# Kernel tuning notes

Hardware: AMD Instinct MI355X
Metric: run time of the kernel (lower is better)

The kernel has to match this reference:

```python
import jax, jax.numpy as jnp
import numpy as np

POOLED = 7          # square pooled grid (grid_width == grid_height required by torch_combined_meshgrid)
NUM_LEVELS = 6      # len_feature_maps; level = clamp(floor(5 + log2(sqrt(w*h))), 0, 5)


def _bilinear_sample(fm, gx, gy):
    """fm: [C, D, D]; gx, gy: [N, G, G] normalized coords in [0,1].
    Faithful to getWeightedSum_ofFourFmapPoints: floor/ceil corner points with
    proportion weights; coord dim 0 (x) indexes fmap rows, dim 1 (y) indexes cols.
    Returns [N, C, G, G]."""
    D = fm.shape[-1]
    ux = gx * (D - 1)
    uy = gy * (D - 1)
    x0 = jnp.floor(ux); x1 = jnp.ceil(ux)
    y0 = jnp.floor(uy); y1 = jnp.ceil(uy)
    ddx = jnp.where(x1 - x0 == 0, 1.0, x1 - x0)
    ddy = jnp.where(y1 - y0 == 0, 1.0, y1 - y0)
    px0 = 1.0 - (ux - x0) / ddx   # proportion_to_take_from_start_x
    px1 = 1.0 - px0
    py0 = 1.0 - (uy - y0) / ddy
    py1 = 1.0 - py0
    ix0 = x0.astype(jnp.int32); ix1 = x1.astype(jnp.int32)
    iy0 = y0.astype(jnp.int32); iy1 = y1.astype(jnp.int32)
    # advanced indexing: fm[:, idx, idx] -> [C, N, G, G]
    tl = fm[:, ix0, iy0]
    tr = fm[:, ix1, iy0]
    bl = fm[:, ix0, iy1]
    br = fm[:, ix1, iy1]
    w_tl = (px0 * py0)[None]
    w_tr = (px1 * py0)[None]
    w_bl = (px0 * py1)[None]
    w_br = (px1 * py1)[None]
    pooled = w_tl * tl + w_tr * tr + w_bl * bl + w_br * br  # [C, N, G, G]
    return jnp.moveaxis(pooled, 0, 1)                        # [N, C, G, G]


def setup_inputs() -> dict:
    key = jax.random.key(0)
    N, C = 2000, 256
    dims = [38, 19, 10, 5, 3, 1]
    kw, kh, kx, ky, *kf = jax.random.split(key, 4 + len(dims))
    w = jax.random.uniform(kw, (N, 1), minval=0.02, maxval=0.98)
    h = jax.random.uniform(kh, (N, 1), minval=0.02, maxval=0.98)
    x1 = jax.random.uniform(kx, (N, 1)) * (1.0 - w)
    y1 = jax.random.uniform(ky, (N, 1)) * (1.0 - h)
    boxes = jnp.concatenate([x1, y1, x1 + w, y1 + h], axis=1)  # x1 y1 x2 y2 in [0,1]
    out = {"boxes": boxes}
    for i, (d, k) in enumerate(zip(dims, kf)):
        out[f"fmap{i}"] = jax.random.normal(k, (1, C, d, d), dtype=jnp.float32)
    return out


def reference(boxes, fmap0, fmap1, fmap2, fmap3, fmap4, fmap5):
    fmaps = [fmap0, fmap1, fmap2, fmap3, fmap4, fmap5]
    N = boxes.shape[0]
    C = fmap0.shape[1]
    G = POOLED
    x1, y1, x2, y2 = boxes[:, 0:1], boxes[:, 1:2], boxes[:, 2:3], boxes[:, 3:4]
    # FPN-style level index: floor(5 + log2(sqrt(w*h))), clamped (constant w.r.t. grad)
    avg = jnp.sqrt((x2 - x1) * (y2 - y1))
    lvl = jnp.clip(jnp.floor((NUM_LEVELS - 1.0) + jnp.log2(avg)), 0, NUM_LEVELS - 1)
    lvl = jax.lax.stop_gradient(lvl.astype(jnp.int32).reshape(-1))  # [N]
    # bilinear interpolation grid: grid[n,i,j] = (x1 + i*dx/(G-1), y1 + j*dy/(G-1)), clamped
    t = jnp.arange(G, dtype=boxes.dtype)
    denom = max(1.0, G - 1.0)
    xr = jnp.clip(x1 + t[None, :] * (x2 - x1) / denom, 0.0, 1.0)  # [N, G]
    yr = jnp.clip(y1 + t[None, :] * (y2 - y1) / denom, 0.0, 1.0)  # [N, G]
    gx = jnp.broadcast_to(xr[:, :, None], (N, G, G))
    gy = jnp.broadcast_to(yr[:, None, :], (N, G, G))
    out = jnp.zeros((N, C, G, G), dtype=fmap0.dtype)
    for l, f in enumerate(fmaps):
        fm = f[0]  # [C, D, D] (single image; one fmap selected per box)
        if fm.shape[-1] == 1:
            # original returns fmap[:, :, 0:1, 0:1]; broadcast the constant to the grid
            pooled = jnp.broadcast_to(fm[None, :, :1, :1], (N, C, G, G))
        else:
            pooled = _bilinear_sample(fm, gx, gy)
        mask = (lvl == l).astype(fmap0.dtype)[:, None, None, None]
        out = out + mask * pooled
    return out
```

## Files before the change

### kernel.cpp

```cpp
#include <hip/hip_runtime.h>

#define G 7
#define CCH 256
#define NLVL 6

__device__ __constant__ int kD[NLVL]  = {38, 19, 10, 5, 3, 1};
__device__ __constant__ int kD2[NLVL] = {1444, 361, 100, 25, 9, 1};
__device__ __constant__ int kBaseT[NLVL + 1] = {0, 369664, 462080, 487680, 494080, 496384, 496640};

#define FMT_TOTAL 496640

__global__ __launch_bounds__(256) void transpose_fmaps(
    const float* __restrict__ f0, const float* __restrict__ f1,
    const float* __restrict__ f2, const float* __restrict__ f3,
    const float* __restrict__ f4, const float* __restrict__ f5,
    float* __restrict__ fmT)
{
    int o = blockIdx.x * blockDim.x + threadIdx.x;
    if (o >= FMT_TOTAL) return;
    int l = 0;
#pragma unroll
    for (int k = 1; k < NLVL; ++k) l += (o >= kBaseT[k]);
    int rel = o - kBaseT[l];
    int p = rel >> 8;
    int c = rel & 255;
    const float* f;
    switch (l) {
        case 0: f = f0; break;
        case 1: f = f1; break;
        case 2: f = f2; break;
        case 3: f = f3; break;
        case 4: f = f4; break;
        default: f = f5; break;
    }
    fmT[o] = f[c * kD2[l] + p];
}

__global__ __launch_bounds__(256) void roialign_main(
    const float* __restrict__ boxes, const float* __restrict__ fmT,
    float* __restrict__ out)
{
    __shared__ float sOut[CCH * 49];
    __shared__ float4 sW[49];
    __shared__ int4 sOff[49];

    int n = blockIdx.x;
    int tid = threadIdx.x;

    if (tid < 49) {
        float bx1 = boxes[n * 4 + 0];
        float by1 = boxes[n * 4 + 1];
        float bx2 = boxes[n * 4 + 2];
        float by2 = boxes[n * 4 + 3];
        float w = bx2 - bx1;
        float h = by2 - by1;
        float avg = sqrtf(w * h);
        float lf = floorf((float)(NLVL - 1) + log2f(avg));
        lf = fminf(fmaxf(lf, 0.0f), (float)(NLVL - 1));
        int lvl = (int)lf;
        int D = kD[lvl];
        float Dm1 = (float)(D - 1);
        int base = kBaseT[lvl];

        int i = tid / 7;
        int j = tid - i * 7;
        float xr = fminf(fmaxf(bx1 + ((float)i * w) / 6.0f, 0.0f), 1.0f);
        float yr = fminf(fmaxf(by1 + ((float)j * h) / 6.0f, 0.0f), 1.0f);
        float ux = xr * Dm1;
        float uy = yr * Dm1;
        float x0 = floorf(ux);
        float y0 = floorf(uy);
        int ix0 = (int)x0;
        int iy0 = (int)y0;
        float fx = ux - x0;
        float fy = uy - y0;
        int ix1 = min(ix0 + 1, D - 1);
        int iy1 = min(iy0 + 1, D - 1);

        sOff[tid] = make_int4(base + (ix0 * D + iy0) * CCH,
                              base + (ix1 * D + iy0) * CCH,
                              base + (ix0 * D + iy1) * CCH,
                              base + (ix1 * D + iy1) * CCH);
        float px0 = 1.0f - fx, py0 = 1.0f - fy;
        sW[tid] = make_float4(px0 * py0, fx * py0, px0 * fy, fx * fy);
    }
    __syncthreads();

#pragma unroll 7
    for (int g = 0; g < 49; ++g) {
        int4 o = sOff[g];
        float4 wv = sW[g];
        float v = wv.x * fmT[o.x + tid] + wv.y * fmT[o.y + tid]
                + wv.z * fmT[o.z + tid] + wv.w * fmT[o.w + tid];
        sOut[tid * 49 + g] = v;
    }

    asm volatile("s_waitcnt lgkmcnt(0)" ::: "memory");
    __builtin_amdgcn_sched_barrier(0);

    int wv_id = tid >> 6;
    int lane = tid & 63;
    const float4* s4 = (const float4*)sOut + wv_id * 784;
    float4* out4 = (float4*)(out + (size_t)n * (CCH * G * G)) + wv_id * 784;
#pragma unroll
    for (int k = 0; k < 12; ++k) {
        out4[k * 64 + lane] = s4[k * 64 + lane];
    }
    if (lane < 16) out4[768 + lane] = s4[768 + lane];
}

__global__ __launch_bounds__(256) void roialign_fallback(
    const float* __restrict__ boxes,
    const float* __restrict__ f0, const float* __restrict__ f1,
    const float* __restrict__ f2, const float* __restrict__ f3,
    const float* __restrict__ f4, const float* __restrict__ f5,
    float* __restrict__ out, int total4)
{
    int t = blockIdx.x * blockDim.x + threadIdx.x;
    if (t >= total4) return;
    const int perN = CCH * G * G;
    int idx = t * 4;
    int n = idx / perN;
    int rem = idx - n * perN;
    float bx1 = boxes[n * 4 + 0], by1 = boxes[n * 4 + 1];
    float bx2 = boxes[n * 4 + 2], by2 = boxes[n * 4 + 3];
    float w = bx2 - bx1, h = by2 - by1;
    float avg = sqrtf(w * h);
    float lf = floorf((float)(NLVL - 1) + log2f(avg));
    lf = fminf(fmaxf(lf, 0.0f), (float)(NLVL - 1));
    int lvl = (int)lf;
    const float* fm;
    switch (lvl) {
        case 0: fm = f0; break;
        case 1: fm = f1; break;
        case 2: fm = f2; break;
        case 3: fm = f3; break;
        case 4: fm = f4; break;
        default: fm = f5; break;
    }
    int D = kD[lvl];
    float Dm1 = (float)(D - 1);
    float4 res;
    float* rp = &res.x;
#pragma unroll
    for (int k = 0; k < 4; ++k) {
        int e = rem + k;
        int j = e % G;
        int iq = e / G;
        int i = iq % G;
        int c = iq / G;
        float xr = fminf(fmaxf(bx1 + ((float)i * w) / 6.0f, 0.0f), 1.0f);
        float yr = fminf(fmaxf(by1 + ((float)j * h) / 6.0f, 0.0f), 1.0f);
        float ux = xr * Dm1, uy = yr * Dm1;
        float x0 = floorf(ux), y0 = floorf(uy);
        int ix0 = (int)x0, iy0 = (int)y0;
        float fx = ux - x0, fy = uy - y0;
        int ix1 = min(ix0 + 1, D - 1), iy1 = min(iy0 + 1, D - 1);
        const float* p = fm + c * D * D;
        float v00 = p[ix0 * D + iy0], v10 = p[ix1 * D + iy0];
        float v01 = p[ix0 * D + iy1], v11 = p[ix1 * D + iy1];
        float px0 = 1.0f - fx, py0 = 1.0f - fy;
        rp[k] = px0 * py0 * v00 + fx * py0 * v10 + px0 * fy * v01 + fx * fy * v11;
    }
    reinterpret_cast<float4*>(out)[t] = res;
}

extern "C" void kernel_launch(void* const* d_in, const int* in_sizes, int n_in,
                              void* d_out, int out_size, void* d_ws, size_t ws_size,
                              hipStream_t stream) {
    const float* boxes = (const float*)d_in[0];
    const float* f0 = (const float*)d_in[1];
    const float* f1 = (const float*)d_in[2];
    const float* f2 = (const float*)d_in[3];
    const float* f3 = (const float*)d_in[4];
    const float* f4 = (const float*)d_in[5];
    const float* f5 = (const float*)d_in[6];
    float* out = (float*)d_out;
    int N = in_sizes[0] / 4;

    if (ws_size >= (size_t)FMT_TOTAL * sizeof(float)) {
        float* fmT = (float*)d_ws;
        transpose_fmaps<<<(FMT_TOTAL + 255) / 256, 256, 0, stream>>>(
            f0, f1, f2, f3, f4, f5, fmT);
        roialign_main<<<N, 256, 0, stream>>>(boxes, fmT, out);
    } else {
        int total4 = out_size / 4;
        roialign_fallback<<<(total4 + 255) / 256, 256, 0, stream>>>(
            boxes, f0, f1, f2, f3, f4, f5, out, total4);
    }
}
```

Before: 34.71 us.

## Make RoIAlign kernel persistent with per-wave setup and deferred output stores

Launches a fixed grid of 512 persistent blocks that loop over boxes instead of one block per box. Each wave now computes its own copy of the sample offsets and weights, which removes the block-wide barrier. The shared-memory store of the previous box is deferred and issued at the top of the next iteration to overlap with the next box's setup. The change risks lower occupancy and load imbalance, since 2000 boxes do not divide evenly across 512 blocks. It also relies on per-wave LDS regions and lgkmcnt waits for correctness instead of __syncthreads.

```diff
diff --git a/kernel.cpp b/kernel.cpp
--- a/kernel.cpp
+++ b/kernel.cpp
@@ -9,6 +9,7 @@
 __device__ __constant__ int kBaseT[NLVL + 1] = {0, 369664, 462080, 487680, 494080, 496384, 496640};
 
 #define FMT_TOTAL 496640
+#define NBLK 512
 
 __global__ __launch_bounds__(256) void transpose_fmaps(
     const float* __restrict__ f0, const float* __restrict__ f1,
@@ -36,77 +37,93 @@
     fmT[o] = f[c * kD2[l] + p];
 }
 
-__global__ __launch_bounds__(256) void roialign_main(
+__global__ __launch_bounds__(256, 2) void roialign_main(
     const float* __restrict__ boxes, const float* __restrict__ fmT,
-    float* __restrict__ out)
+    float* __restrict__ out, int N)
 {
-    __shared__ float sOut[CCH * 49];
-    __shared__ float4 sW[49];
-    __shared__ int4 sOff[49];
-
-    int n = blockIdx.x;
+    __shared__ float  sOut[CCH * 49];
+    __shared__ int4   sOffT[4 * 49];
+    __shared__ float4 sWT[4 * 49];
+
     int tid = threadIdx.x;
-
-    if (tid < 49) {
-        float bx1 = boxes[n * 4 + 0];
-        float by1 = boxes[n * 4 + 1];
-        float bx2 = boxes[n * 4 + 2];
-        float by2 = boxes[n * 4 + 3];
-        float w = bx2 - bx1;
-        float h = by2 - by1;
-        float avg = sqrtf(w * h);
-        float lf = floorf((float)(NLVL - 1) + log2f(avg));
-        lf = fminf(fmaxf(lf, 0.0f), (float)(NLVL - 1));
-        int lvl = (int)lf;
-        int D = kD[lvl];
-        float Dm1 = (float)(D - 1);
-        int base = kBaseT[lvl];
-
-        int i = tid / 7;
-        int j = tid - i * 7;
-        float xr = fminf(fmaxf(bx1 + ((float)i * w) / 6.0f, 0.0f), 1.0f);
-        float yr = fminf(fmaxf(by1 + ((float)j * h) / 6.0f, 0.0f), 1.0f);
-        float ux = xr * Dm1;
-        float uy = yr * Dm1;
-        float x0 = floorf(ux);
-        float y0 = floorf(uy);
-        int ix0 = (int)x0;
-        int iy0 = (int)y0;
-        float fx = ux - x0;
-        float fy = uy - y0;
-        int ix1 = min(ix0 + 1, D - 1);
-        int iy1 = min(iy0 + 1, D - 1);
-
-        sOff[tid] = make_int4(base + (ix0 * D + iy0) * CCH,
-                              base + (ix1 * D + iy0) * CCH,
-                              base + (ix0 * D + iy1) * CCH,
-                              base + (ix1 * D + iy1) * CCH);
-        float px0 = 1.0f - fx, py0 = 1.0f - fy;
-        sW[tid] = make_float4(px0 * py0, fx * py0, px0 * fy, fx * fy);
-    }
-    __syncthreads();
+    int wv = tid >> 6;
+    int lane = tid & 63;
+
+    int4*   offT = sOffT + wv * 49;
+    float4* wT   = sWT + wv * 49;
+    const float4* s4 = (const float4*)sOut + wv * 784;
+
+    int havePrev = 0;
+    size_t prevBase = 0;
+
+    for (int n = blockIdx.x; n < N; n += NBLK) {
+        if (havePrev) {
+            float4* o4 = (float4*)(out + prevBase) + wv * 784;
+#pragma unroll
+            for (int k = 0; k < 12; ++k) o4[k * 64 + lane] = s4[k * 64 + lane];
+            if (lane < 16) o4[768 + lane] = s4[768 + lane];
+        }
+
+        if (lane < 49) {
+            float bx1 = boxes[n * 4 + 0];
+            float by1 = boxes[n * 4 + 1];
+            float bx2 = boxes[n * 4 + 2];
+            float by2 = boxes[n * 4 + 3];
+            float w = bx2 - bx1;
+            float h = by2 - by1;
+            float avg = sqrtf(w * h);
+            float lf = floorf((float)(NLVL - 1) + log2f(avg));
+            lf = fminf(fmaxf(lf, 0.0f), (float)(NLVL - 1));
+            int lvl = (int)lf;
+            int D = kD[lvl];
+            float Dm1 = (float)(D - 1);
+            int base = kBaseT[lvl];
+
+            int i = lane / 7;
+            int j = lane - i * 7;
+            float xr = fminf(fmaxf(bx1 + ((float)i * w) / 6.0f, 0.0f), 1.0f);
+            float yr = fminf(fmaxf(by1 + ((float)j * h) / 6.0f, 0.0f), 1.0f);
+            float ux = xr * Dm1;
+            float uy = yr * Dm1;
+            float x0 = floorf(ux);
+            float y0 = floorf(uy);
+            int ix0 = (int)x0;
+            int iy0 = (int)y0;
+            float fx = ux - x0;
+            float fy = uy - y0;
+            int ix1 = min(ix0 + 1, D - 1);
+            int iy1 = min(iy0 + 1, D - 1);
+
+            offT[lane] = make_int4(base + (ix0 * D + iy0) * CCH,
+                                   base + (ix1 * D + iy0) * CCH,
+                                   base + (ix0 * D + iy1) * CCH,
+                                   base + (ix1 * D + iy1) * CCH);
+            float px0 = 1.0f - fx, py0 = 1.0f - fy;
+            wT[lane] = make_float4(px0 * py0, fx * py0, px0 * fy, fx * fy);
+        }
+        asm volatile("s_waitcnt lgkmcnt(0)" ::: "memory");
+        __builtin_amdgcn_sched_barrier(0);
 
 #pragma unroll 7
-    for (int g = 0; g < 49; ++g) {
-        int4 o = sOff[g];
-        float4 wv = sW[g];
-        float v = wv.x * fmT[o.x + tid] + wv.y * fmT[o.y + tid]
-                + wv.z * fmT[o.z + tid] + wv.w * fmT[o.w + tid];
-        sOut[tid * 49 + g] = v;
-    }
-
-    asm volatile("s_waitcnt lgkmcnt(0)" ::: "memory");
-    __builtin_amdgcn_sched_barrier(0);
-
-    int wv_id = tid >> 6;
-    int lane = tid & 63;
-    const float4* s4 = (const float4*)sOut + wv_id * 784;
-    float4* out4 = (float4*)(out + (size_t)n * (CCH * G * G)) + wv_id * 784;
-#pragma unroll
-    for (int k = 0; k < 12; ++k) {
-        out4[k * 64 + lane] = s4[k * 64 + lane];
-    }
-    if (lane < 16) out4[768 + lane] = s4[768 + lane];
+        for (int g = 0; g < 49; ++g) {
+            int4 o = offT[g];
+            float4 wv4 = wT[g];
+            float v = wv4.x * fmT[o.x + tid] + wv4.y * fmT[o.y + tid]
+                    + wv4.z * fmT[o.z + tid] + wv4.w * fmT[o.w + tid];
+            sOut[tid * 49 + g] = v;
+        }
+
+        havePrev = 1;
+        prevBase = (size_t)n * (CCH * G * G);
+    }
+
+    if (havePrev) {
+        asm volatile("s_waitcnt lgkmcnt(0)" ::: "memory");
+        float4* o4 = (float4*)(out + prevBase) + wv * 784;
+#pragma unroll
+        for (int k = 0; k < 12; ++k) o4[k * 64 + lane] = s4[k * 64 + lane];
+        if (lane < 16) o4[768 + lane] = s4[768 + lane];
+    }
 }
 
 __global__ __launch_bounds__(256) void roialign_fallback(
@@ -182,7 +199,7 @@
         float* fmT = (float*)d_ws;
         transpose_fmaps<<<(FMT_TOTAL + 255) / 256, 256, 0, stream>>>(
             f0, f1, f2, f3, f4, f5, fmT);
-        roialign_main<<<N, 256, 0, stream>>>(boxes, fmT, out);
+        roialign_main<<<NBLK, 256, 0, stream>>>(boxes, fmT, out, N);
     } else {
         int total4 = out_size / 4;
         roialign_fallback<<<(total4 + 255) / 256, 256, 0, stream>>>(
```

New measurement: 38.74 us. 11.6% more time.

## Deduplicate identical bilinear corner sets per box and prefetch next slot

Applied to the files above, without the earlier changes.

Grid points that share the same floor cell (common on coarse levels) are grouped with wave-level shuffles and ballots, so each unique corner set's four feature loads are issued once and reused for all points in the group. The next slot's loads are software-prefetched while the current group is written. This cuts redundant global and L2 loads but adds serial shuffle and ballot loops in the setup phase and a data-dependent inner loop with less unrolling.

```diff
diff --git a/kernel.cpp b/kernel.cpp
--- a/kernel.cpp
+++ b/kernel.cpp
@@ -40,14 +40,17 @@
     const float* __restrict__ boxes, const float* __restrict__ fmT,
     float* __restrict__ out)
 {
-    __shared__ float sOut[CCH * 49];
+    __shared__ float  sOut[CCH * 49];
     __shared__ float4 sW[49];
-    __shared__ int4 sOff[49];
+    __shared__ int4   sOffSlot[49];
+    __shared__ unsigned long long sMask[49];
+    __shared__ int    sK;
 
     int n = blockIdx.x;
     int tid = threadIdx.x;
 
     if (tid < 49) {
+        int g = tid;
         float bx1 = boxes[n * 4 + 0];
         float by1 = boxes[n * 4 + 1];
         float bx2 = boxes[n * 4 + 2];
@@ -62,8 +65,8 @@
         float Dm1 = (float)(D - 1);
         int base = kBaseT[lvl];
 
-        int i = tid / 7;
-        int j = tid - i * 7;
+        int i = g / 7;
+        int j = g - i * 7;
         float xr = fminf(fmaxf(bx1 + ((float)i * w) / 6.0f, 0.0f), 1.0f);
         float yr = fminf(fmaxf(by1 + ((float)j * h) / 6.0f, 0.0f), 1.0f);
         float ux = xr * Dm1;
@@ -77,22 +80,51 @@
         int ix1 = min(ix0 + 1, D - 1);
         int iy1 = min(iy0 + 1, D - 1);
 
-        sOff[tid] = make_int4(base + (ix0 * D + iy0) * CCH,
-                              base + (ix1 * D + iy0) * CCH,
-                              base + (ix0 * D + iy1) * CCH,
-                              base + (ix1 * D + iy1) * CCH);
         float px0 = 1.0f - fx, py0 = 1.0f - fy;
-        sW[tid] = make_float4(px0 * py0, fx * py0, px0 * fy, fx * fy);
+        sW[g] = make_float4(px0 * py0, fx * py0, px0 * fy, fx * fy);
+
+        int key = (ix0 << 6) | iy0;
+        int firstIdx = g;
+        for (int p = 48; p >= 0; --p) {
+            int kp = __shfl(key, p);
+            if (p < g && kp == key) firstIdx = p;
+        }
+        unsigned long long firstMask = __ballot(firstIdx == g);
+        int slot = __popcll(firstMask & ((1ull << firstIdx) - 1));
+
+        for (int f = 0; f < 49; ++f) {
+            unsigned long long m = __ballot(firstIdx == f);
+            if (g == f && firstIdx == g) sMask[slot] = m;
+        }
+        if (firstIdx == g) {
+            sOffSlot[slot] = make_int4(base + (ix0 * D + iy0) * CCH,
+                                       base + (ix1 * D + iy0) * CCH,
+                                       base + (ix0 * D + iy1) * CCH,
+                                       base + (ix1 * D + iy1) * CCH);
+        }
+        if (g == 0) sK = (int)__popcll(firstMask);
     }
     __syncthreads();
 
-#pragma unroll 7
-    for (int g = 0; g < 49; ++g) {
-        int4 o = sOff[g];
-        float4 wv = sW[g];
-        float v = wv.x * fmT[o.x + tid] + wv.y * fmT[o.y + tid]
-                + wv.z * fmT[o.z + tid] + wv.w * fmT[o.w + tid];
-        sOut[tid * 49 + g] = v;
+    int Kl = sK;
+    int4 o0 = sOffSlot[0];
+    float a0 = fmT[o0.x + tid], a1 = fmT[o0.y + tid];
+    float a2 = fmT[o0.z + tid], a3 = fmT[o0.w + tid];
+    for (int s = 0; s < Kl; ++s) {
+        float b0 = a0, b1 = a1, b2 = a2, b3 = a3;
+        unsigned long long m = sMask[s];
+        if (s + 1 < Kl) {
+            int4 o2 = sOffSlot[s + 1];
+            a0 = fmT[o2.x + tid]; a1 = fmT[o2.y + tid];
+            a2 = fmT[o2.z + tid]; a3 = fmT[o2.w + tid];
+        }
+        while (m) {
+            int g = __builtin_ctzll(m);
+            m &= m - 1;
+            float4 wv4 = sW[g];
+            sOut[tid * 49 + g] = wv4.x * b0 + wv4.y * b1
+                               + wv4.z * b2 + wv4.w * b3;
+        }
     }
 
     asm volatile("s_waitcnt lgkmcnt(0)" ::: "memory");
```

Result: slower. 45.26 us (+30.4%).

## Precompute per-box sample offset/weight tables in separate kernel

Applied to the files above, without the earlier changes.

Moves the per-box level selection and bilinear offset/weight computation out of the main ROIAlign kernel into a new make_tables kernel that writes a global table. The main kernel then reads the uniform table entries directly (likely scalar loads), with no serial prologue or __syncthreads, and the gather loop is fully unrolled. The cost is an extra kernel launch plus a table write and read of about 3 MB, and a larger workspace requirement, so the fast path may fall back if the workspace is too small.

```diff
diff --git a/kernel.cpp b/kernel.cpp
--- a/kernel.cpp
+++ b/kernel.cpp
@@ -9,6 +9,10 @@
 __device__ __constant__ int kBaseT[NLVL + 1] = {0, 369664, 462080, 487680, 494080, 496384, 496640};
 
 #define FMT_TOTAL 496640
+#define TBL_BYTES_PER (32)
+#define WS_NEEDED (FMT_TOTAL * 4 + 2000 * 49 * TBL_BYTES_PER)
+
+struct BoxTab { int4 o; float4 w; };
 
 __global__ __launch_bounds__(256) void transpose_fmaps(
     const float* __restrict__ f0, const float* __restrict__ f1,
@@ -36,62 +40,70 @@
     fmT[o] = f[c * kD2[l] + p];
 }
 
+__global__ __launch_bounds__(256) void make_tables(
+    const float* __restrict__ boxes, BoxTab* __restrict__ tbl, int total)
+{
+    int t = blockIdx.x * blockDim.x + threadIdx.x;
+    if (t >= total) return;
+    int n = t / 49;
+    int g = t - n * 49;
+
+    float bx1 = boxes[n * 4 + 0];
+    float by1 = boxes[n * 4 + 1];
+    float bx2 = boxes[n * 4 + 2];
+    float by2 = boxes[n * 4 + 3];
+    float w = bx2 - bx1;
+    float h = by2 - by1;
+    float avg = sqrtf(w * h);
+    float lf = floorf((float)(NLVL - 1) + log2f(avg));
+    lf = fminf(fmaxf(lf, 0.0f), (float)(NLVL - 1));
+    int lvl = (int)lf;
+    int D = kD[lvl];
+    float Dm1 = (float)(D - 1);
+    int base = kBaseT[lvl];
+
+    int i = g / 7;
+    int j = g - i * 7;
+    float xr = fminf(fmaxf(bx1 + ((float)i * w) / 6.0f, 0.0f), 1.0f);
+    float yr = fminf(fmaxf(by1 + ((float)j * h) / 6.0f, 0.0f), 1.0f);
+    float ux = xr * Dm1;
+    float uy = yr * Dm1;
+    float x0 = floorf(ux);
+    float y0 = floorf(uy);
+    int ix0 = (int)x0;
+    int iy0 = (int)y0;
+    float fx = ux - x0;
+    float fy = uy - y0;
+    int ix1 = min(ix0 + 1, D - 1);
+    int iy1 = min(iy0 + 1, D - 1);
+
+    BoxTab bt;
+    bt.o = make_int4(base + (ix0 * D + iy0) * CCH,
+                     base + (ix1 * D + iy0) * CCH,
+                     base + (ix0 * D + iy1) * CCH,
+                     base + (ix1 * D + iy1) * CCH);
+    float px0 = 1.0f - fx, py0 = 1.0f - fy;
+    bt.w = make_float4(px0 * py0, fx * py0, px0 * fy, fx * fy);
+    tbl[t] = bt;
+}
+
 __global__ __launch_bounds__(256) void roialign_main(
-    const float* __restrict__ boxes, const float* __restrict__ fmT,
+    const BoxTab* __restrict__ tbl, const float* __restrict__ fmT,
     float* __restrict__ out)
 {
     __shared__ float sOut[CCH * 49];
-    __shared__ float4 sW[49];
-    __shared__ int4 sOff[49];
 
     int n = blockIdx.x;
     int tid = threadIdx.x;
 
-    if (tid < 49) {
-        float bx1 = boxes[n * 4 + 0];
-        float by1 = boxes[n * 4 + 1];
-        float bx2 = boxes[n * 4 + 2];
-        float by2 = boxes[n * 4 + 3];
-        float w = bx2 - bx1;
-        float h = by2 - by1;
-        float avg = sqrtf(w * h);
-        float lf = floorf((float)(NLVL - 1) + log2f(avg));
-        lf = fminf(fmaxf(lf, 0.0f), (float)(NLVL - 1));
-        int lvl = (int)lf;
-        int D = kD[lvl];
-        float Dm1 = (float)(D - 1);
-        int base = kBaseT[lvl];
-
-        int i = tid / 7;
-        int j = tid - i * 7;
-        float xr = fminf(fmaxf(bx1 + ((float)i * w) / 6.0f, 0.0f), 1.0f);
-        float yr = fminf(fmaxf(by1 + ((float)j * h) / 6.0f, 0.0f), 1.0f);
-        float ux = xr * Dm1;
-        float uy = yr * Dm1;
-        float x0 = floorf(ux);
-        float y0 = floorf(uy);
-        int ix0 = (int)x0;
-        int iy0 = (int)y0;
-        float fx = ux - x0;
-        float fy = uy - y0;
-        int ix1 = min(ix0 + 1, D - 1);
-        int iy1 = min(iy0 + 1, D - 1);
-
-        sOff[tid] = make_int4(base + (ix0 * D + iy0) * CCH,
-                              base + (ix1 * D + iy0) * CCH,
-                              base + (ix0 * D + iy1) * CCH,
-                              base + (ix1 * D + iy1) * CCH);
-        float px0 = 1.0f - fx, py0 = 1.0f - fy;
-        sW[tid] = make_float4(px0 * py0, fx * py0, px0 * fy, fx * fy);
-    }
-    __syncthreads();
-
-#pragma unroll 7
+    const BoxTab* bt = tbl + n * 49;
+
+#pragma unroll
     for (int g = 0; g < 49; ++g) {
-        int4 o = sOff[g];
-        float4 wv = sW[g];
-        float v = wv.x * fmT[o.x + tid] + wv.y * fmT[o.y + tid]
-                + wv.z * fmT[o.z + tid] + wv.w * fmT[o.w + tid];
+        int4   o  = bt[g].o;
+        float4 w4 = bt[g].w;
+        float v = w4.x * fmT[o.x + tid] + w4.y * fmT[o.y + tid]
+                + w4.z * fmT[o.z + tid] + w4.w * fmT[o.w + tid];
         sOut[tid * 49 + g] = v;
     }
 
@@ -178,11 +190,15 @@
     float* out = (float*)d_out;
     int N = in_sizes[0] / 4;
 
-    if (ws_size >= (size_t)FMT_TOTAL * sizeof(float)) {
+    size_t needed = (size_t)FMT_TOTAL * 4 + (size_t)N * 49 * TBL_BYTES_PER;
+    if (ws_size >= needed) {
         float* fmT = (float*)d_ws;
+        BoxTab* tbl = (BoxTab*)((char*)d_ws + (size_t)FMT_TOTAL * 4);
         transpose_fmaps<<<(FMT_TOTAL + 255) / 256, 256, 0, stream>>>(
             f0, f1, f2, f3, f4, f5, fmT);
-        roialign_main<<<N, 256, 0, stream>>>(boxes, fmT, out);
+        int total = N * 49;
+        make_tables<<<(total + 255) / 256, 256, 0, stream>>>(boxes, tbl, total);
+        roialign_main<<<N, 256, 0, stream>>>(tbl, fmT, out);
     } else {
         int total4 = out_size / 4;
         roialign_fallback<<<(total4 + 255) / 256, 256, 0, stream>>>(
```

Result: slower. 43.49 us (+25.3%).
